# Kernel optimization log

Hardware: AMD Instinct MI355X
Metric: run time of the kernel (lower is better)

The kernel has to match this reference:

```python
import jax, jax.numpy as jnp
import numpy as np


def setup_inputs() -> dict:
    key0 = jax.random.key(0)
    kq, kk, kv, km = jax.random.split(key0, 4)
    B, H, S, Dk = 2, 16, 2048, 64
    query = jax.random.normal(kq, (B, H, S, Dk), dtype=jnp.float32)
    key = jax.random.normal(kk, (B, H, S, Dk), dtype=jnp.float32)
    value = jax.random.normal(kv, (B, H, S, Dk), dtype=jnp.float32)
    mask = jax.random.randint(km, (B, 1, 1, S), 0, 2, dtype=jnp.int32)
    return {"query": query, "key": key, "value": value, "mask": mask}


def reference(query, key, value, mask):
    d_k = query.shape[-1]
    scale = 1.0 / jnp.sqrt(jnp.asarray(d_k, dtype=query.dtype))
    # scores: [B, H, Sq, Sk]
    scores = jnp.einsum("bhqd,bhkd->bhqk", query, key) * scale
    scores = jnp.where(mask == 0, jnp.asarray(-1e9, dtype=scores.dtype), scores)
    attention_weights = jax.nn.softmax(scores, axis=-1)
    output = jnp.einsum("bhqk,bhkd->bhqd", attention_weights, value)
    return output, attention_weights
```

## Files before the change

### kernel.cpp

```cpp
#include <hip/hip_runtime.h>
#include <stdint.h>

#define S_LEN 2048
#define DK 64
#define MT 64
#define NT 64
#define LD 72

typedef __attribute__((ext_vector_type(8))) short bf16x8;
typedef __attribute__((ext_vector_type(4))) float floatx4;
typedef __attribute__((ext_vector_type(16))) float f32x16;
typedef __attribute__((ext_vector_type(2))) unsigned int uint2v;

__device__ inline unsigned short f2bf(float f) {
    union { float f; unsigned u; } v; v.f = f;
    unsigned r = v.u + 0x7FFFu + ((v.u >> 16) & 1u);
    return (unsigned short)(r >> 16);
}

__device__ inline void async16(const void* g, void* l) {
    using gu32 = const __attribute__((address_space(1))) unsigned int;
    using lu32 = __attribute__((address_space(3))) unsigned int;
    gu32* gp = reinterpret_cast<gu32*>(reinterpret_cast<uintptr_t>(g));
    lu32* lp = reinterpret_cast<lu32*>(static_cast<unsigned int>(reinterpret_cast<uintptr_t>(l)));
    __builtin_amdgcn_global_load_lds(gp, lp, 16, 0, 0);
}

__device__ inline unsigned swz(unsigned o) { return o ^ ((o >> 3) & 0x70u); }

__device__ inline void stage8k(const char* g, char* l, int wave, int lane) {
    const unsigned o0 = (unsigned)(wave * 2048 + lane * 16);
    async16(g + swz(o0), l + o0);
    async16(g + swz(o0 + 1024), l + o0 + 1024);
}

__device__ inline void stageV(const char* Vh, int kt, char* l, int wave, int lane) {
    const unsigned o0 = (unsigned)(wave * 2048 + lane * 16);
    #pragma unroll
    for (int j = 0; j < 2; ++j) {
        const unsigned o = o0 + j * 1024;
        const unsigned s = swz(o);
        async16(Vh + (size_t)(o >> 7) * 4096 + kt * 128 + (s & 127), l + o);
    }
}

__global__ __launch_bounds__(256) void convert_qk(
    const float* __restrict__ Q, const float* __restrict__ K,
    unsigned short* __restrict__ Qb, unsigned short* __restrict__ Kb)
{
    int i = blockIdx.x * 256 + threadIdx.x;
    const int NQ = (2 * 16 * 2048 * 64) / 4;
    const float* src; unsigned short* dst; int j; float sc;
    if (i < NQ) { src = Q; dst = Qb; j = i; sc = 0.125f; }
    else        { src = K; dst = Kb; j = i - NQ; sc = 1.0f; }
    float4 f = ((const float4*)src)[j];
    ushort4 o;
    o.x = f2bf(f.x * sc); o.y = f2bf(f.y * sc);
    o.z = f2bf(f.z * sc); o.w = f2bf(f.w * sc);
    ((ushort4*)dst)[j] = o;
}

__global__ __launch_bounds__(256) void transpose_v(
    const float* __restrict__ V, unsigned short* __restrict__ Vt)
{
    __shared__ unsigned short t[64][72];
    const int head = blockIdx.y, kt = blockIdx.x, tid = threadIdx.x;
    const float* src = V + ((size_t)head * S_LEN + kt * 64) * DK;
    {
        const int r = tid >> 2, c = (tid & 3) * 16;
        #pragma unroll
        for (int i = 0; i < 4; ++i) {
            float4 f = *(const float4*)(src + r * DK + c + i * 4);
            t[r][c + i * 4 + 0] = f2bf(f.x);
            t[r][c + i * 4 + 1] = f2bf(f.y);
            t[r][c + i * 4 + 2] = f2bf(f.z);
            t[r][c + i * 4 + 3] = f2bf(f.w);
        }
    }
    __syncthreads();
    {
        const int d = tid >> 2, kb = (tid & 3) * 16;
        unsigned short tmp[16];
        #pragma unroll
        for (int j = 0; j < 16; ++j) tmp[j] = t[kb + j][d];
        unsigned short* dst = Vt + (size_t)head * DK * S_LEN + (size_t)d * S_LEN + kt * 64 + kb;
        ((uint4*)dst)[0] = *(const uint4*)&tmp[0];
        ((uint4*)dst)[1] = *(const uint4*)&tmp[8];
    }
}

__global__ __launch_bounds__(256) void sdpa_main(
    const unsigned short* __restrict__ Qb, const unsigned short* __restrict__ Kb,
    const unsigned short* __restrict__ Vt, const int* __restrict__ mask,
    float* __restrict__ O, float* __restrict__ W)
{
    __shared__ alignas(16) char lds[32768];
    __shared__ float red[4][32];

    const int tid  = threadIdx.x;
    const int wave = tid >> 6;
    const int lane = tid & 63;
    const int l31  = lane & 31;
    const int hi   = lane >> 5;
    const int qg   = wave >> 1;
    const int kb   = wave & 1;

    const int head = blockIdx.y;
    const int bidx = head >> 4;
    const int q0   = blockIdx.x * MT;

    const char* Qh = (const char*)(Qb + ((size_t)head * S_LEN + q0) * DK);
    const char* Kh = (const char*)(Kb + (size_t)head * S_LEN * DK);
    const char* Vh = (const char*)(Vt + (size_t)head * DK * S_LEN);
    const int*  mk = mask + bidx * S_LEN;
    float* Wh = W + (size_t)head * S_LEN * S_LEN;
    float* Oh = O + (size_t)head * S_LEN * DK;

    char* B0 = lds;
    char* B1 = lds + 8192;
    char* B2 = lds + 16384;
    char* B3 = lds + 24576;

    stage8k(Qh, B0, wave, lane);
    stage8k(Kh, B1, wave, lane);
    __syncthreads();

    bf16x8 qf[4];
    {
        const unsigned rq = (unsigned)(qg * 32 + l31) * 128;
        #pragma unroll
        for (int m = 0; m < 4; ++m)
            qf[m] = *(const bf16x8*)(B0 + swz(rq + m * 32 + hi * 16));
    }

    const unsigned rk = (unsigned)(kb * 32 + l31) * 128;

    float lsum = 0.f;
    for (int t = 0; t < 32; ++t) {
        char* cur = (t & 1) ? B2 : B1;
        if (t < 31) stage8k(Kh + (size_t)(t + 1) * 8192, (t & 1) ? B1 : B2, wave, lane);
        const unsigned long long mm = __ballot(mk[t * 64 + lane] != 0);
        const unsigned mw = (unsigned)(mm >> (kb * 32));
        f32x16 z;
        #pragma unroll
        for (int r = 0; r < 16; ++r) z[r] = 0.f;
        #pragma unroll
        for (int m = 0; m < 4; ++m) {
            bf16x8 kf = *(const bf16x8*)(cur + swz(rk + m * 32 + hi * 16));
            z = __builtin_amdgcn_mfma_f32_32x32x16_bf16(kf, qf[m], z, 0, 0, 0);
        }
        #pragma unroll
        for (int r = 0; r < 16; ++r) {
            const int kl = (r & 3) + 8 * (r >> 2) + 4 * hi;
            lsum += ((mw >> kl) & 1u) ? __expf(z[r]) : 0.f;
        }
        __syncthreads();
    }
    lsum += __shfl_xor(lsum, 32);
    if (hi == 0) red[wave][l31] = lsum;
    __syncthreads();
    const float rl = 1.0f / (red[qg * 2][l31] + red[qg * 2 + 1][l31]);

    f32x16 oacc0, oacc1;
    #pragma unroll
    for (int r = 0; r < 16; ++r) { oacc0[r] = 0.f; oacc1[r] = 0.f; }

    stage8k(Kh, B0, wave, lane);
    stageV(Vh, 0, B2, wave, lane);
    __syncthreads();

    for (int t = 0; t < 32; ++t) {
        char* curK = (t & 1) ? B1 : B0;
        char* curV = (t & 1) ? B3 : B2;
        if (t < 31) {
            stage8k(Kh + (size_t)(t + 1) * 8192, (t & 1) ? B0 : B1, wave, lane);
            stageV(Vh, t + 1, (t & 1) ? B2 : B3, wave, lane);
        }
        const unsigned long long mm = __ballot(mk[t * 64 + lane] != 0);
        const unsigned mw = (unsigned)(mm >> (kb * 32));

        f32x16 z;
        #pragma unroll
        for (int r = 0; r < 16; ++r) z[r] = 0.f;
        #pragma unroll
        for (int m = 0; m < 4; ++m) {
            bf16x8 kf = *(const bf16x8*)(curK + swz(rk + m * 32 + hi * 16));
            z = __builtin_amdgcn_mfma_f32_32x32x16_bf16(kf, qf[m], z, 0, 0, 0);
        }
        #pragma unroll
        for (int r = 0; r < 16; ++r) {
            const int kl = (r & 3) + 8 * (r >> 2) + 4 * hi;
            const float e = __expf(z[r]) * rl;
            z[r] = ((mw >> kl) & 1u) ? e : 0.f;
        }
        {
            float* wp = Wh + (size_t)(q0 + qg * 32 + l31) * S_LEN + t * 64 + kb * 32 + 4 * hi;
            #pragma unroll
            for (int g = 0; g < 4; ++g)
                *(float4*)(wp + 8 * g) = make_float4(z[4*g], z[4*g+1], z[4*g+2], z[4*g+3]);
        }
        unsigned pk0[4], pk1[4];
        #pragma unroll
        for (int g = 0; g < 4; ++g) {
            pk0[g] = (unsigned)f2bf(z[4*g+0]) | ((unsigned)f2bf(z[4*g+1]) << 16);
            pk1[g] = (unsigned)f2bf(z[4*g+2]) | ((unsigned)f2bf(z[4*g+3]) << 16);
        }
        #pragma unroll
        for (int m2 = 0; m2 < 2; ++m2) {
            uint2v s0 = __builtin_amdgcn_permlane32_swap(pk0[2*m2], pk0[2*m2+1], false, false);
            uint2v s1 = __builtin_amdgcn_permlane32_swap(pk1[2*m2], pk1[2*m2+1], false, false);
            union { unsigned u[4]; bf16x8 v; } pa;
            pa.u[0] = s0[0]; pa.u[1] = s1[0]; pa.u[2] = s0[1]; pa.u[3] = s1[1];
            const unsigned cv = (unsigned)(kb * 64 + m2 * 32 + hi * 16);
            bf16x8 v0 = *(const bf16x8*)(curV + swz((unsigned)l31 * 128 + cv));
            bf16x8 v1 = *(const bf16x8*)(curV + swz((unsigned)(32 + l31) * 128 + cv));
            oacc0 = __builtin_amdgcn_mfma_f32_32x32x16_bf16(v0, pa.v, oacc0, 0, 0, 0);
            oacc1 = __builtin_amdgcn_mfma_f32_32x32x16_bf16(v1, pa.v, oacc1, 0, 0, 0);
        }
        __syncthreads();
    }

    float* redO = (float*)lds;
    if (kb == 1) {
        float* dst = redO + (size_t)(qg * 64 + lane) * 32;
        #pragma unroll
        for (int r = 0; r < 16; ++r) { dst[r] = oacc0[r]; dst[16 + r] = oacc1[r]; }
    }
    __syncthreads();
    if (kb == 0) {
        const float* sp = redO + (size_t)(qg * 64 + lane) * 32;
        #pragma unroll
        for (int r = 0; r < 16; ++r) { oacc0[r] += sp[r]; oacc1[r] += sp[16 + r]; }
        float* op = Oh + (size_t)(q0 + qg * 32 + l31) * DK + 4 * hi;
        #pragma unroll
        for (int g = 0; g < 4; ++g) {
            *(float4*)(op + 8 * g)      = make_float4(oacc0[4*g], oacc0[4*g+1], oacc0[4*g+2], oacc0[4*g+3]);
            *(float4*)(op + 32 + 8 * g) = make_float4(oacc1[4*g], oacc1[4*g+1], oacc1[4*g+2], oacc1[4*g+3]);
        }
    }
}

__global__ __launch_bounds__(256) void sdpa_fb(
    const float* __restrict__ Q, const float* __restrict__ K,
    const float* __restrict__ V, const int* __restrict__ mask,
    float* __restrict__ O, float* __restrict__ W)
{
    __shared__ alignas(16) unsigned short qs[MT * LD];
    __shared__ alignas(16) unsigned short ks[NT * LD];
    __shared__ alignas(16) unsigned short vs[DK * LD];
    __shared__ alignas(16) unsigned short ps[MT * LD];
    __shared__ float addm[NT];

    const int tid = threadIdx.x, wave = tid >> 6, lane = tid & 63;
    const int quad = lane >> 4, l16 = lane & 15;
    const int head = blockIdx.y, bidx = head >> 4, q0 = blockIdx.x * MT;

    const float* Qh = Q + (size_t)head * S_LEN * DK;
    const float* Kh = K + (size_t)head * S_LEN * DK;
    const float* Vh = V + (size_t)head * S_LEN * DK;
    const int* mk = mask + bidx * S_LEN;
    float* Wh = W + (size_t)head * S_LEN * S_LEN;
    float* Oh = O + (size_t)head * S_LEN * DK;

    #pragma unroll
    for (int i = 0; i < 4; ++i) {
        const int g = i * 256 + tid, row = g >> 4, col = (g & 15) * 4;
        float4 f = *(const float4*)(Qh + (size_t)(q0 + row) * DK + col);
        unsigned* d = (unsigned*)&qs[row * LD + col];
        d[0] = f2bf(f.x) | ((unsigned)f2bf(f.y) << 16);
        d[1] = f2bf(f.z) | ((unsigned)f2bf(f.w) << 16);
    }
    __syncthreads();
    const bf16x8 qa0 = *(const bf16x8*)&qs[(wave * 16 + l16) * LD + quad * 8];
    const bf16x8 qa1 = *(const bf16x8*)&qs[(wave * 16 + l16) * LD + 32 + quad * 8];

    float m[4], l[4];
    #pragma unroll
    for (int r = 0; r < 4; ++r) { m[r] = -1e30f; l[r] = 0.0f; }

    for (int kt = 0; kt < S_LEN / NT; ++kt) {
        #pragma unroll
        for (int i = 0; i < 4; ++i) {
            const int g = i * 256 + tid, row = g >> 4, col = (g & 15) * 4;
            float4 f = *(const float4*)(Kh + (size_t)(kt * NT + row) * DK + col);
            unsigned* d = (unsigned*)&ks[row * LD + col];
            d[0] = f2bf(f.x) | ((unsigned)f2bf(f.y) << 16);
            d[1] = f2bf(f.z) | ((unsigned)f2bf(f.w) << 16);
        }
        if (tid < NT) addm[tid] = mk[kt * NT + tid] ? 0.0f : -1e30f;
        __syncthreads();
        floatx4 acc[4];
        #pragma unroll
        for (int c = 0; c < 4; ++c) {
            bf16x8 b0 = *(const bf16x8*)&ks[(c * 16 + l16) * LD + quad * 8];
            bf16x8 b1 = *(const bf16x8*)&ks[(c * 16 + l16) * LD + 32 + quad * 8];
            floatx4 z = {0.f, 0.f, 0.f, 0.f};
            z = __builtin_amdgcn_mfma_f32_16x16x32_bf16(qa0, b0, z, 0, 0, 0);
            z = __builtin_amdgcn_mfma_f32_16x16x32_bf16(qa1, b1, z, 0, 0, 0);
            acc[c] = z;
        }
        float sv[4][4];
        #pragma unroll
        for (int c = 0; c < 4; ++c) {
            float am = addm[c * 16 + l16];
            #pragma unroll
            for (int r = 0; r < 4; ++r) sv[c][r] = acc[c][r] * 0.125f + am;
        }
        #pragma unroll
        for (int r = 0; r < 4; ++r) {
            float tmax = fmaxf(fmaxf(sv[0][r], sv[1][r]), fmaxf(sv[2][r], sv[3][r]));
            #pragma unroll
            for (int off = 1; off < 16; off <<= 1) tmax = fmaxf(tmax, __shfl_xor(tmax, off, 64));
            float mn = fmaxf(m[r], tmax);
            float ts = __expf(sv[0][r] - mn) + __expf(sv[1][r] - mn)
                     + __expf(sv[2][r] - mn) + __expf(sv[3][r] - mn);
            #pragma unroll
            for (int off = 1; off < 16; off <<= 1) ts += __shfl_xor(ts, off, 64);
            l[r] = l[r] * __expf(m[r] - mn) + ts;
            m[r] = mn;
        }
        __syncthreads();
    }
    float rl[4];
    #pragma unroll
    for (int r = 0; r < 4; ++r) rl[r] = 1.0f / l[r];

    floatx4 oacc[4];
    #pragma unroll
    for (int c = 0; c < 4; ++c) oacc[c] = (floatx4){0.f, 0.f, 0.f, 0.f};

    for (int kt = 0; kt < S_LEN / NT; ++kt) {
        #pragma unroll
        for (int i = 0; i < 4; ++i) {
            const int g = i * 256 + tid, row = g >> 4, col = (g & 15) * 4;
            float4 f = *(const float4*)(Kh + (size_t)(kt * NT + row) * DK + col);
            unsigned* d = (unsigned*)&ks[row * LD + col];
            d[0] = f2bf(f.x) | ((unsigned)f2bf(f.y) << 16);
            d[1] = f2bf(f.z) | ((unsigned)f2bf(f.w) << 16);
        }
        {
            const int row = tid >> 2, colg = (tid & 3) << 4;
            const float4* vsrc = (const float4*)(Vh + (size_t)(kt * NT + row) * DK + colg);
            #pragma unroll
            for (int i = 0; i < 4; ++i) {
                float4 f = vsrc[i];
                const int dbase = colg + i * 4;
                vs[(dbase + 0) * LD + row] = f2bf(f.x);
                vs[(dbase + 1) * LD + row] = f2bf(f.y);
                vs[(dbase + 2) * LD + row] = f2bf(f.z);
                vs[(dbase + 3) * LD + row] = f2bf(f.w);
            }
        }
        if (tid < NT) addm[tid] = mk[kt * NT + tid] ? 0.0f : -1e30f;
        __syncthreads();
        floatx4 acc[4];
        #pragma unroll
        for (int c = 0; c < 4; ++c) {
            bf16x8 b0 = *(const bf16x8*)&ks[(c * 16 + l16) * LD + quad * 8];
            bf16x8 b1 = *(const bf16x8*)&ks[(c * 16 + l16) * LD + 32 + quad * 8];
            floatx4 z = {0.f, 0.f, 0.f, 0.f};
            z = __builtin_amdgcn_mfma_f32_16x16x32_bf16(qa0, b0, z, 0, 0, 0);
            z = __builtin_amdgcn_mfma_f32_16x16x32_bf16(qa1, b1, z, 0, 0, 0);
            acc[c] = z;
        }
        #pragma unroll
        for (int c = 0; c < 4; ++c) {
            float am = addm[c * 16 + l16];
            #pragma unroll
            for (int r = 0; r < 4; ++r) {
                const int lrow = wave * 16 + quad * 4 + r;
                float w = __expf(acc[c][r] * 0.125f + am - m[r]) * rl[r];
                Wh[(size_t)(q0 + lrow) * S_LEN + kt * NT + c * 16 + l16] = w;
                ps[lrow * LD + c * 16 + l16] = f2bf(w);
            }
        }
        __syncthreads();
        bf16x8 pa0 = *(const bf16x8*)&ps[(wave * 16 + l16) * LD + quad * 8];
        bf16x8 pa1 = *(const bf16x8*)&ps[(wave * 16 + l16) * LD + 32 + quad * 8];
        #pragma unroll
        for (int c = 0; c < 4; ++c) {
            bf16x8 v0 = *(const bf16x8*)&vs[(c * 16 + l16) * LD + quad * 8];
            bf16x8 v1 = *(const bf16x8*)&vs[(c * 16 + l16) * LD + 32 + quad * 8];
            oacc[c] = __builtin_amdgcn_mfma_f32_16x16x32_bf16(pa0, v0, oacc[c], 0, 0, 0);
            oacc[c] = __builtin_amdgcn_mfma_f32_16x16x32_bf16(pa1, v1, oacc[c], 0, 0, 0);
        }
        __syncthreads();
    }
    #pragma unroll
    for (int c = 0; c < 4; ++c) {
        #pragma unroll
        for (int r = 0; r < 4; ++r) {
            const int lrow = wave * 16 + quad * 4 + r;
            Oh[(size_t)(q0 + lrow) * DK + c * 16 + l16] = oacc[c][r];
        }
    }
}

extern "C" void kernel_launch(void* const* d_in, const int* in_sizes, int n_in,
                              void* d_out, int out_size, void* d_ws, size_t ws_size,
                              hipStream_t stream) {
    const float* Q  = (const float*)d_in[0];
    const float* K  = (const float*)d_in[1];
    const float* V  = (const float*)d_in[2];
    const int* mask = (const int*)d_in[3];

    float* O = (float*)d_out;
    float* W = (float*)d_out + (size_t)2 * 16 * 2048 * 64;

    const size_t elems = (size_t)2 * 16 * 2048 * 64;
    const size_t need  = 3 * elems * sizeof(unsigned short);

    if (ws_size >= need) {
        unsigned short* Qb = (unsigned short*)d_ws;
        unsigned short* Kb = Qb + elems;
        unsigned short* Vt = Kb + elems;
        convert_qk<<<dim3((2 * elems / 4) / 256), 256, 0, stream>>>(Q, K, Qb, Kb);
        transpose_v<<<dim3(32, 32), 256, 0, stream>>>(V, Vt);
        sdpa_main<<<dim3(S_LEN / MT, 32), 256, 0, stream>>>(Qb, Kb, Vt, mask, O, W);
    } else {
        sdpa_fb<<<dim3(S_LEN / MT, 32), 256, 0, stream>>>(Q, K, V, mask, O, W);
    }
}
```

Baseline: 716.7 us.

## Precompute mask bitwords in LDS and pipeline loads with explicit vmcnt waits

Mask bits are packed once per block into shared-memory words, which removes the per-tile global mask load and ballot. The full __syncthreads at the end of each tile is replaced by explicit s_waitcnt vmcnt(N) plus raw s_barrier, so the next K/V tile's async loads can stay in flight while the current tile computes. LDS buffers are rotated to fit this schedule, and s_setprio brackets the MFMA sections. The approach depends on exact vmcnt counts matching the number of loads issued by stage8k/stageV, which is fragile: a wrong count would read stale LDS data.

```diff
diff --git a/kernel.cpp b/kernel.cpp
--- a/kernel.cpp
+++ b/kernel.cpp
@@ -96,6 +96,7 @@
 {
     __shared__ alignas(16) char lds[32768];
     __shared__ float red[4][32];
+    __shared__ unsigned mwords[64];
 
     const int tid  = threadIdx.x;
     const int wave = tid >> 6;
@@ -123,6 +124,13 @@
 
     stage8k(Qh, B0, wave, lane);
     stage8k(Kh, B1, wave, lane);
+    if (tid < 64) {
+        const int* mb = mk + tid * 32;
+        unsigned w = 0;
+        #pragma unroll
+        for (int i = 0; i < 32; ++i) w |= (mb[i] != 0 ? 1u : 0u) << i;
+        mwords[tid] = w;
+    }
     __syncthreads();
 
     bf16x8 qf[4];
@@ -138,23 +146,30 @@
     float lsum = 0.f;
     for (int t = 0; t < 32; ++t) {
         char* cur = (t & 1) ? B2 : B1;
-        if (t < 31) stage8k(Kh + (size_t)(t + 1) * 8192, (t & 1) ? B1 : B2, wave, lane);
-        const unsigned long long mm = __ballot(mk[t * 64 + lane] != 0);
-        const unsigned mw = (unsigned)(mm >> (kb * 32));
+        if (t < 31) {
+            stage8k(Kh + (size_t)(t + 1) * 8192, (t & 1) ? B1 : B2, wave, lane);
+            asm volatile("s_waitcnt vmcnt(2)" ::: "memory");
+        } else {
+            asm volatile("s_waitcnt vmcnt(0)" ::: "memory");
+        }
+        __builtin_amdgcn_s_barrier();
+        const unsigned mw = mwords[t * 2 + kb];
         f32x16 z;
         #pragma unroll
         for (int r = 0; r < 16; ++r) z[r] = 0.f;
+        __builtin_amdgcn_s_setprio(1);
         #pragma unroll
         for (int m = 0; m < 4; ++m) {
             bf16x8 kf = *(const bf16x8*)(cur + swz(rk + m * 32 + hi * 16));
             z = __builtin_amdgcn_mfma_f32_32x32x16_bf16(kf, qf[m], z, 0, 0, 0);
         }
+        __builtin_amdgcn_s_setprio(0);
         #pragma unroll
         for (int r = 0; r < 16; ++r) {
             const int kl = (r & 3) + 8 * (r >> 2) + 4 * hi;
             lsum += ((mw >> kl) & 1u) ? __expf(z[r]) : 0.f;
         }
-        __syncthreads();
+        __builtin_amdgcn_s_barrier();
     }
     lsum += __shfl_xor(lsum, 32);
     if (hi == 0) red[wave][l31] = lsum;
@@ -165,28 +180,32 @@
     #pragma unroll
     for (int r = 0; r < 16; ++r) { oacc0[r] = 0.f; oacc1[r] = 0.f; }
 
-    stage8k(Kh, B0, wave, lane);
-    stageV(Vh, 0, B2, wave, lane);
-    __syncthreads();
+    stage8k(Kh, B1, wave, lane);
+    stageV(Vh, 0, B0, wave, lane);
 
     for (int t = 0; t < 32; ++t) {
-        char* curK = (t & 1) ? B1 : B0;
-        char* curV = (t & 1) ? B3 : B2;
+        char* curK = (t & 1) ? B2 : B1;
+        char* curV = (t & 1) ? B3 : B0;
         if (t < 31) {
-            stage8k(Kh + (size_t)(t + 1) * 8192, (t & 1) ? B0 : B1, wave, lane);
-            stageV(Vh, t + 1, (t & 1) ? B2 : B3, wave, lane);
-        }
-        const unsigned long long mm = __ballot(mk[t * 64 + lane] != 0);
-        const unsigned mw = (unsigned)(mm >> (kb * 32));
-
+            stage8k(Kh + (size_t)(t + 1) * 8192, (t & 1) ? B1 : B2, wave, lane);
+            stageV(Vh, t + 1, (t & 1) ? B0 : B3, wave, lane);
+        }
+        if (t == 0)      asm volatile("s_waitcnt vmcnt(4)" ::: "memory");
+        else if (t < 31) asm volatile("s_waitcnt vmcnt(8)" ::: "memory");
+        else             asm volatile("s_waitcnt vmcnt(4)" ::: "memory");
+        __builtin_amdgcn_s_barrier();
+
+        const unsigned mw = mwords[t * 2 + kb];
         f32x16 z;
         #pragma unroll
         for (int r = 0; r < 16; ++r) z[r] = 0.f;
+        __builtin_amdgcn_s_setprio(1);
         #pragma unroll
         for (int m = 0; m < 4; ++m) {
             bf16x8 kf = *(const bf16x8*)(curK + swz(rk + m * 32 + hi * 16));
             z = __builtin_amdgcn_mfma_f32_32x32x16_bf16(kf, qf[m], z, 0, 0, 0);
         }
+        __builtin_amdgcn_s_setprio(0);
         #pragma unroll
         for (int r = 0; r < 16; ++r) {
             const int kl = (r & 3) + 8 * (r >> 2) + 4 * hi;
@@ -205,6 +224,7 @@
             pk0[g] = (unsigned)f2bf(z[4*g+0]) | ((unsigned)f2bf(z[4*g+1]) << 16);
             pk1[g] = (unsigned)f2bf(z[4*g+2]) | ((unsigned)f2bf(z[4*g+3]) << 16);
         }
+        __builtin_amdgcn_s_setprio(1);
         #pragma unroll
         for (int m2 = 0; m2 < 2; ++m2) {
             uint2v s0 = __builtin_amdgcn_permlane32_swap(pk0[2*m2], pk0[2*m2+1], false, false);
@@ -217,9 +237,11 @@
             oacc0 = __builtin_amdgcn_mfma_f32_32x32x16_bf16(v0, pa.v, oacc0, 0, 0, 0);
             oacc1 = __builtin_amdgcn_mfma_f32_32x32x16_bf16(v1, pa.v, oacc1, 0, 0, 0);
         }
-        __syncthreads();
-    }
-
+        __builtin_amdgcn_s_setprio(0);
+        __builtin_amdgcn_s_barrier();
+    }
+
+    __syncthreads();
     float* redO = (float*)lds;
     if (kb == 1) {
         float* dst = redO + (size_t)(qg * 64 + lane) * 32;
```

After: 727.2 us. About the same (+1.5%).
